# Optimization experiments

Measured on AMD Instinct MI355X. Metric: run time of the kernel, lower is better.

Reference implementation:

```python
import jax, jax.numpy as jnp
import numpy as np
import math

TEMP = 0.07
BASE_TEMP = 0.07
M = 0.2
S = 10.0
COS_M = math.cos(M)
SIN_M = math.sin(M)
TH = math.cos(math.pi - M)
MM = math.sin(math.pi - M) * M
N_CLASSES = 2793
EPS = 1e-12


def _l2norm_rows(x):
    # F.normalize(x, p=2, dim=1)
    n = jnp.linalg.norm(x, axis=1, keepdims=True)
    return x / jnp.maximum(n, EPS)


def setup_inputs() -> dict:
    key = jax.random.key(0)
    k1, k2, k3, k4 = jax.random.split(key, 4)
    bsz, n_views, d = 1024, 2, 192
    return {
        "features": jax.random.normal(k1, (bsz, n_views, d), jnp.float32),
        "labels": jax.random.randint(k2, (bsz,), 0, N_CLASSES),
        "fc_w": jax.random.normal(k3, (N_CLASSES, d), jnp.float32) * 0.05,
        "fc_b": jax.random.normal(k4, (N_CLASSES,), jnp.float32) * 0.01,
    }


def reference(features, labels, fc_w, fc_b):
    bsz, n_views, d = features.shape
    n = bsz * n_views  # 2048 (must be <= N_CLASSES for the one_hot scatter)

    # supervised mask from labels: mask[i,j] = 1 if same class
    mask = (labels[:, None] == labels[None, :]).astype(jnp.float32)  # [bsz,bsz]

    # contrast_feature = cat(unbind(features, dim=1), dim=0), then L2-normalized
    cf = jnp.concatenate([features[:, v] for v in range(n_views)], axis=0)  # [n,d]
    cf = _l2norm_rows(cf)
    anchor = cf  # contrast_mode == 'all'

    x_norm = jnp.maximum(jnp.linalg.norm(cf, axis=1, keepdims=True), 1e-12)
    x = cf / x_norm
    w_norm = jnp.maximum(jnp.linalg.norm(anchor, axis=1, keepdims=True), 1e-12)
    w = anchor / w_norm

    cosine = x @ w.T                      # [n,n]
    cosine = _l2norm_rows(cosine)         # row L2-normalize (as in source)
    sine = jnp.sqrt(jnp.clip(1.0 - cosine * cosine, 0.0, 1.0))
    phi = cosine * COS_M - sine * SIN_M
    phi = jnp.where(cosine - TH > 0, phi, cosine - MM)
    output = S * phi                      # [n,n]

    attlabels = jnp.concatenate([labels, labels])  # [n]

    # h2 @ one_hot where one_hot[j,k] = 1 iff j < n and attlabels[j] == k
    # => (h2 @ one_hot)[i,k] = sum_{j<n, attlabels[j]==k} h2[i,j]
    h2 = jnp.tanh(cf @ fc_w.T + fc_b)     # [n, N_CLASSES]
    seg = jax.ops.segment_sum(h2[:, :n].T, attlabels, num_segments=N_CLASSES)  # [C,n]
    denominator = jnp.exp(seg.T)          # [n, N_CLASSES]; zero cols -> exp(0)=1

    # vectorized form of per-row python loop: a_i = den[i, attlabels[i]] / sum(den[i])
    num = jnp.take_along_axis(denominator, attlabels[:, None], axis=1)[:, 0]  # [n]
    a = num / denominator.sum(axis=1)     # [n]
    # F.normalize on [n,1]: each row divided by its own |a| -> sign(a) (here all 1)
    atten = a / jnp.maximum(jnp.abs(a), EPS)  # [n]
    # A = min(expand(atten), expand(atten)) == atten broadcast along rows
    A = atten[:, None]                    # [n,1], broadcasts over columns

    anchor_dot_contrast = output / TEMP
    logits_max = jax.lax.stop_gradient(anchor_dot_contrast.max(axis=1, keepdims=True))
    logits = (anchor_dot_contrast - logits_max) * A

    mask_full = jnp.tile(mask, (n_views, n_views))            # [n,n]
    logits_mask = 1.0 - jnp.eye(n, dtype=jnp.float32)          # zero diagonal
    mask_full = mask_full * logits_mask

    exp_logits = jnp.exp(logits) * logits_mask
    log_prob = logits - jnp.log(exp_logits.sum(axis=1, keepdims=True))
    mean_log_prob_pos = (mask_full * log_prob).sum(axis=1) / mask_full.sum(axis=1)

    loss = -(TEMP / BASE_TEMP) * mean_log_prob_pos
    return loss.reshape(n_views, bsz).mean()
```

## Files before the change

### kernel.cpp

```cpp
#include <hip/hip_runtime.h>

typedef __attribute__((ext_vector_type(8))) _Float16 half8;
typedef __attribute__((ext_vector_type(4))) float f32x4;

#define COS_M 0.98006657784124163f
#define SIN_M 0.19866933079506122f
#define TH_C  (-0.98006657784124163f)
#define MM_C  0.039733866159012244f
#define S_OVER_TEMP (10.0f / 0.07f)

__device__ inline float xform(float c) {
  float s2 = fmaxf(1.0f - c * c, 0.0f);
  float sn = sqrtf(s2);
  float phi = c * COS_M - sn * SIN_M;
  float out = (c - TH_C > 0.0f) ? phi : (c - MM_C);
  return out * S_OVER_TEMP;
}

__global__ __launch_bounds__(256) void k_gemm_norm(const float* __restrict__ feats,
                                                   _Float16* __restrict__ Gh) {
  __shared__ alignas(16) _Float16 la[128 * 200];
  __shared__ alignas(16) _Float16 lb[128 * 200];
  __shared__ float rsA[128], rsBs[128];
  const int bm = blockIdx.x, bn = blockIdx.y;
  const int t = threadIdx.x;
  const bool diag = (bn == bm);

  auto stage = [&](int bt, _Float16* lds, float* rs) {
    const int rr = t >> 1, h = t & 1;
    const int r = bt * 128 + rr;
    const float4* s4 =
        (const float4*)(feats + (size_t)((r & 1023) * 2 + (r >> 10)) * 192 + h * 96);
    float ss = 0.f;
    _Float16* dst = lds + rr * 200 + h * 96;
#pragma unroll
    for (int q = 0; q < 12; ++q) {
      float4 va = s4[2 * q], vb = s4[2 * q + 1];
      ss += va.x * va.x + va.y * va.y + va.z * va.z + va.w * va.w;
      ss += vb.x * vb.x + vb.y * vb.y + vb.z * vb.z + vb.w * vb.w;
      half8 o = {(_Float16)va.x, (_Float16)va.y, (_Float16)va.z, (_Float16)va.w,
                 (_Float16)vb.x, (_Float16)vb.y, (_Float16)vb.z, (_Float16)vb.w};
      *(half8*)(dst + q * 8) = o;
    }
    ss += __shfl_xor(ss, 1);
    if (h == 0) rs[rr] = rsqrtf(fmaxf(ss, 1e-24f));
  };
  stage(bm, la, rsA);
  if (!diag) stage(bn, lb, rsBs);
  __syncthreads();
  const _Float16* Bp = diag ? la : lb;
  const float* rsB = diag ? rsA : rsBs;

  const int lane = t & 63;
  const int w = t >> 6;
  const int wr = w >> 1, wc = w & 1;
  const int lr = lane & 15, kg = lane >> 4;

  f32x4 acc[4][4];
#pragma unroll
  for (int m = 0; m < 4; ++m)
#pragma unroll
    for (int n = 0; n < 4; ++n) acc[m][n] = (f32x4){0.f, 0.f, 0.f, 0.f};

#pragma unroll
  for (int kc = 0; kc < 6; ++kc) {
    half8 af[4], bf[4];
    const int koff = kc * 32 + kg * 8;
#pragma unroll
    for (int m = 0; m < 4; ++m)
      af[m] = *(const half8*)&la[(wr * 64 + m * 16 + lr) * 200 + koff];
#pragma unroll
    for (int n = 0; n < 4; ++n)
      bf[n] = *(const half8*)&Bp[(wc * 64 + n * 16 + lr) * 200 + koff];
#pragma unroll
    for (int m = 0; m < 4; ++m)
#pragma unroll
      for (int n = 0; n < 4; ++n)
        acc[m][n] = __builtin_amdgcn_mfma_f32_16x16x32_f16(af[m], bf[n], acc[m][n], 0, 0, 0);
  }

  const int rb = bm * 128 + wr * 64;
  const int cb = bn * 128 + wc * 64;
#pragma unroll
  for (int m = 0; m < 4; ++m)
#pragma unroll
    for (int n = 0; n < 4; ++n) {
      const int r0 = rb + m * 16 + kg * 4;
      const int c0 = cb + n * 16 + lr;
      const float sb = rsB[wc * 64 + n * 16 + lr];
#pragma unroll
      for (int e = 0; e < 4; ++e) {
        const float sa = rsA[wr * 64 + m * 16 + kg * 4 + e];
        Gh[(size_t)(r0 + e) * 2048 + c0] = (_Float16)(acc[m][n][e] * sa * sb);
      }
    }
}

__global__ __launch_bounds__(64) void k_rowloss(const _Float16* __restrict__ Gh,
                                                const int* __restrict__ labels,
                                                float* __restrict__ lossv) {
  const int i = blockIdx.x;
  const int l = threadIdx.x;
  const _Float16* row = Gh + (size_t)i * 2048;

  half8 v[4];
#pragma unroll
  for (int p = 0; p < 4; ++p)
    v[p] = *(const half8*)&row[512 * p + 8 * l];

  float gv[4][8];
#pragma unroll
  for (int p = 0; p < 4; ++p)
#pragma unroll
    for (int u = 0; u < 8; ++u) gv[p][u] = (float)v[p][u];

  float ss = 0.f, mx = -3.4e38f;
#pragma unroll
  for (int p = 0; p < 4; ++p)
#pragma unroll
    for (int u = 0; u < 8; ++u) { ss += gv[p][u] * gv[p][u]; mx = fmaxf(mx, gv[p][u]); }
#pragma unroll
  for (int o = 32; o; o >>= 1) {
    ss += __shfl_xor(ss, o);
    mx = fmaxf(mx, __shfl_xor(mx, o));
  }
  const float invn = 1.0f / fmaxf(sqrtf(ss), 1e-12f);
  const float Mst = xform(mx * invn);

  const int4 a0 = *(const int4*)&labels[8 * l];
  const int4 a1 = *(const int4*)&labels[8 * l + 4];
  const int4 b0 = *(const int4*)&labels[512 + 8 * l];
  const int4 b1 = *(const int4*)&labels[512 + 8 * l + 4];
  const int labs[2][8] = {{a0.x, a0.y, a0.z, a0.w, a1.x, a1.y, a1.z, a1.w},
                          {b0.x, b0.y, b0.z, b0.w, b1.x, b1.y, b1.z, b1.w}};
  const int mylab = labels[i & 1023];

  float es = 0.f, ps = 0.f, cn = 0.f;
#pragma unroll
  for (int p = 0; p < 4; ++p)
#pragma unroll
    for (int u = 0; u < 8; ++u) {
      const int j = 512 * p + 8 * l + u;
      const float lg = xform(gv[p][u] * invn) - Mst;
      if (j != i) {
        es += expf(lg);
        if (labs[p & 1][u] == mylab) { ps += lg; cn += 1.f; }
      }
    }
#pragma unroll
  for (int o = 32; o; o >>= 1) {
    es += __shfl_xor(es, o);
    ps += __shfl_xor(ps, o);
    cn += __shfl_xor(cn, o);
  }
  if (l == 0) lossv[i] = -(ps / cn - logf(es));
}

__global__ __launch_bounds__(256) void k_final(const float* __restrict__ lossv,
                                               float* __restrict__ out) {
  const int t = threadIdx.x;
  float s = 0.f;
  for (int j = t; j < 2048; j += 256) s += lossv[j];
#pragma unroll
  for (int o = 32; o; o >>= 1) s += __shfl_down(s, o);
  __shared__ float r4[4];
  if ((t & 63) == 0) r4[t >> 6] = s;
  __syncthreads();
  if (t == 0) out[0] = (r4[0] + r4[1] + r4[2] + r4[3]) * (1.0f / 2048.0f);
}

extern "C" void kernel_launch(void* const* d_in, const int* in_sizes, int n_in,
                              void* d_out, int out_size, void* d_ws, size_t ws_size,
                              hipStream_t stream) {
  const float* feats = (const float*)d_in[0];
  const int* labels = (const int*)d_in[1];

  char* ws = (char*)d_ws;
  float* lossv = (float*)ws;
  _Float16* Gh = (_Float16*)(ws + (1 << 20));

  dim3 g2(16, 16);
  k_gemm_norm<<<g2, 256, 0, stream>>>(feats, Gh);
  k_rowloss<<<2048, 64, 0, stream>>>(Gh, labels, lossv);
  k_final<<<1, 256, 0, stream>>>(lossv, (float*)d_out);
}
```

Measured before the change: 29.13 us.

## Compute per-row sum-of-squares and max partials in GEMM epilogue

The GEMM epilogue now reduces each 64-column strip of the fp32 Gram tile into per-row partial sum-of-squares and max values, written to workspace. The row-loss kernel sums 32 partials instead of reducing the fp16 row, and packs four rows per 256-thread block instead of one row per 64-thread block. This removes a cross-lane reduction pass from the loss kernel and computes the norm from fp32 values before fp16 rounding. In exchange it adds shuffle reductions and scattered partial stores to the GEMM, plus 64 strided scalar loads per row in the loss kernel.

```diff
diff --git a/kernel.cpp b/kernel.cpp
--- a/kernel.cpp
+++ b/kernel.cpp
@@ -18,7 +18,9 @@
 }
 
 __global__ __launch_bounds__(256) void k_gemm_norm(const float* __restrict__ feats,
-                                                   _Float16* __restrict__ Gh) {
+                                                   _Float16* __restrict__ Gh,
+                                                   float* __restrict__ ssp,
+                                                   float* __restrict__ mxp) {
   __shared__ alignas(16) _Float16 la[128 * 200];
   __shared__ alignas(16) _Float16 lb[128 * 200];
   __shared__ float rsA[128], rsBs[128];
@@ -81,6 +83,7 @@
 
   const int rb = bm * 128 + wr * 64;
   const int cb = bn * 128 + wc * 64;
+  const int grp = bn * 2 + wc;
 #pragma unroll
   for (int m = 0; m < 4; ++m)
 #pragma unroll
@@ -94,13 +97,41 @@
         Gh[(size_t)(r0 + e) * 2048 + c0] = (_Float16)(acc[m][n][e] * sa * sb);
       }
     }
-}
-
-__global__ __launch_bounds__(64) void k_rowloss(const _Float16* __restrict__ Gh,
-                                                const int* __restrict__ labels,
-                                                float* __restrict__ lossv) {
-  const int i = blockIdx.x;
-  const int l = threadIdx.x;
+
+#pragma unroll
+  for (int m = 0; m < 4; ++m) {
+#pragma unroll
+    for (int e = 0; e < 4; ++e) {
+      const float sa = rsA[wr * 64 + m * 16 + kg * 4 + e];
+      float s = 0.f, x = -3.4e38f;
+#pragma unroll
+      for (int n = 0; n < 4; ++n) {
+        const float g = acc[m][n][e] * sa * rsB[wc * 64 + n * 16 + lr];
+        s += g * g;
+        x = fmaxf(x, g);
+      }
+#pragma unroll
+      for (int mk = 1; mk < 16; mk <<= 1) {
+        s += __shfl_xor(s, mk);
+        x = fmaxf(x, __shfl_xor(x, mk));
+      }
+      if (lr == 0) {
+        const int row = rb + m * 16 + kg * 4 + e;
+        ssp[grp * 2048 + row] = s;
+        mxp[grp * 2048 + row] = x;
+      }
+    }
+  }
+}
+
+__global__ __launch_bounds__(256) void k_rowloss(const _Float16* __restrict__ Gh,
+                                                 const float* __restrict__ ssp,
+                                                 const float* __restrict__ mxp,
+                                                 const int* __restrict__ labels,
+                                                 float* __restrict__ lossv) {
+  const int w = threadIdx.x >> 6;
+  const int i = blockIdx.x * 4 + w;
+  const int l = threadIdx.x & 63;
   const _Float16* row = Gh + (size_t)i * 2048;
 
   half8 v[4];
@@ -108,21 +139,11 @@
   for (int p = 0; p < 4; ++p)
     v[p] = *(const half8*)&row[512 * p + 8 * l];
 
-  float gv[4][8];
-#pragma unroll
-  for (int p = 0; p < 4; ++p)
-#pragma unroll
-    for (int u = 0; u < 8; ++u) gv[p][u] = (float)v[p][u];
-
   float ss = 0.f, mx = -3.4e38f;
 #pragma unroll
-  for (int p = 0; p < 4; ++p)
-#pragma unroll
-    for (int u = 0; u < 8; ++u) { ss += gv[p][u] * gv[p][u]; mx = fmaxf(mx, gv[p][u]); }
-#pragma unroll
-  for (int o = 32; o; o >>= 1) {
-    ss += __shfl_xor(ss, o);
-    mx = fmaxf(mx, __shfl_xor(mx, o));
+  for (int q = 0; q < 32; ++q) {
+    ss += ssp[q * 2048 + i];
+    mx = fmaxf(mx, mxp[q * 2048 + i]);
   }
   const float invn = 1.0f / fmaxf(sqrtf(ss), 1e-12f);
   const float Mst = xform(mx * invn);
@@ -141,7 +162,7 @@
 #pragma unroll
     for (int u = 0; u < 8; ++u) {
       const int j = 512 * p + 8 * l + u;
-      const float lg = xform(gv[p][u] * invn) - Mst;
+      const float lg = xform((float)v[p][u] * invn) - Mst;
       if (j != i) {
         es += expf(lg);
         if (labs[p & 1][u] == mylab) { ps += lg; cn += 1.f; }
@@ -177,10 +198,12 @@
 
   char* ws = (char*)d_ws;
   float* lossv = (float*)ws;
+  float* ssp   = (float*)(ws + 16384);
+  float* mxp   = (float*)(ws + 16384 + 262144);
   _Float16* Gh = (_Float16*)(ws + (1 << 20));
 
   dim3 g2(16, 16);
-  k_gemm_norm<<<g2, 256, 0, stream>>>(feats, Gh);
-  k_rowloss<<<2048, 64, 0, stream>>>(Gh, labels, lossv);
+  k_gemm_norm<<<g2, 256, 0, stream>>>(feats, Gh, ssp, mxp);
+  k_rowloss<<<512, 256, 0, stream>>>(Gh, ssp, mxp, labels, lossv);
   k_final<<<1, 256, 0, stream>>>(lossv, (float*)d_out);
 }
```

Result: slower. 33.53 us (+15.1%).
